# Performance work log

Hardware: AMD Instinct MI355X
Metric: run time of the kernel (lower is better)

## Reference

```python
import jax, jax.numpy as jnp
import numpy as np
import math

VOCAB, D, L, NC, DC, K, DFF = 50257, 1024, 8, 4096, 256, 8, 4096
B, T = 8, 256

def ternary_ste(w):
    # torch: w_q + (w - w_q).detach() -> forward value == w, grad only via w_q
    alpha = jnp.maximum(jnp.mean(jnp.abs(w)), 1e-5)
    w_q = jnp.clip(jnp.round(w / alpha), -1.0, 1.0)
    return w_q + jax.lax.stop_gradient(w - w_q)

def rmsnorm(x, w):
    return x * jax.lax.rsqrt(jnp.mean(x * x, axis=-1, keepdims=True) + 1e-6) * w

def setup_inputs() -> dict:
    key = jax.random.key(0)
    ks = jax.random.split(key, 16)
    n = lambda k, sh, s: (jax.random.normal(k, sh, dtype=jnp.float32) * s)
    return {
        'tokens': jax.random.randint(ks[0], (B, T), 0, VOCAB),
        'embed': n(ks[1], (VOCAB, D), 0.02),
        'ln_in_w': jnp.ones((D,), jnp.float32),
        'ln_out_w': jnp.ones((D,), jnp.float32),
        'W_route': n(ks[2], (L, NC, D), 0.02),
        'cells': n(ks[3], (L, NC, DC), 0.01),
        'W_in': n(ks[4], (L, D, DC), 0.01),
        'W_out': n(ks[5], (L, DC, D), 0.01),
        'state_decay': jnp.full((L,), 3.0, jnp.float32),
        'state_gate_w': jnp.full((L, D), 0.1, jnp.float32),
        'state_gate_b': jnp.zeros((L, D), jnp.float32),
        'state_scale': jnp.full((L, D), 0.1, jnp.float32),
        'cell_scale': jnp.full((L,), 0.1, jnp.float32),
        'W_ff_gate': n(ks[6], (L, D, DFF), 0.02),
        'W_ff_up': n(ks[7], (L, D, DFF), 0.02),
        'W_ff_down': n(ks[8], (L, DFF, D), 0.02),
        'ff_norm_w': jnp.ones((L, D), jnp.float32),
        'norm_w': jnp.ones((L, D), jnp.float32),
    }

def _layer(x, Wr, cells, Wi, Wo, sd, sgw, sgb, ss, cs, Wg, Wu, Wd, ffn_w, nrm_w):
    Bx, Tx, Dx = x.shape
    # cell memory
    scores = jnp.einsum('btd,cd->btc', x, ternary_ste(Wr)) / math.sqrt(Dx)
    topk_s, topk_i = jax.lax.top_k(scores, K)          # [B,T,K]
    w = jax.nn.softmax(topk_s, axis=-1)
    cell_vals = cells[topk_i]                          # [B,T,K,DC]
    readout = jnp.einsum('btkc,btk->btc', cell_vals, w)
    x_in = jnp.einsum('btd,dc->btc', x, ternary_ste(Wi))
    cell_out = jnp.einsum('btc,cd->btd', readout + x_in, ternary_ste(Wo))
    # running state scan
    gate = jax.nn.sigmoid(x * sgw + sgb)
    updates = gate * x                                  # [B,T,D]
    decay = jnp.clip(jax.nn.sigmoid(sd), 0.01, 0.99)
    def step(h, u):
        h = h * decay + u
        return h, h
    _, states = jax.lax.scan(step, jnp.zeros((Bx, Dx), x.dtype), jnp.swapaxes(updates, 0, 1))
    state_out = jnp.swapaxes(states, 0, 1) * ss
    x = rmsnorm(x + cs * cell_out + state_out, nrm_w)
    # ternary SwiGLU FFN
    h = rmsnorm(x, ffn_w)
    g = jnp.einsum('btd,df->btf', h, ternary_ste(Wg))
    u = jnp.einsum('btd,df->btf', h, ternary_ste(Wu))
    ff = jnp.einsum('btf,fd->btd', jax.nn.silu(g) * u, ternary_ste(Wd))
    return x + ff

def reference(tokens, embed, ln_in_w, ln_out_w, W_route, cells, W_in, W_out,
              state_decay, state_gate_w, state_gate_b, state_scale, cell_scale,
              W_ff_gate, W_ff_up, W_ff_down, ff_norm_w, norm_w):
    h = rmsnorm(embed[tokens], ln_in_w)
    for i in range(L):
        h = _layer(h, W_route[i], cells[i], W_in[i], W_out[i], state_decay[i],
                   state_gate_w[i], state_gate_b[i], state_scale[i], cell_scale[i],
                   W_ff_gate[i], W_ff_up[i], W_ff_down[i], ff_norm_w[i], norm_w[i])
    logits = jnp.einsum('btd,vd->btv', rmsnorm(h, ln_out_w), embed)  # tied head
    return logits
```

## Files before the change

kernel.cpp:

```cpp
#include <hip/hip_runtime.h>
#include <stdint.h>

typedef __attribute__((ext_vector_type(8))) short bf16x8;
typedef __attribute__((ext_vector_type(4))) float f32x4;
typedef unsigned short u16;
typedef unsigned int u32;

#define MTOK 2048
#define DMODEL 1024
#define NCELL 4096
#define DCELL 256
#define DFF 4096
#define NVOCAB 50257
#define VPAD_LD 50304

static __device__ __forceinline__ u16 f2bf(float f) {
  u32 u = __builtin_bit_cast(u32, f);
  u = (u + 0x7FFFu + ((u >> 16) & 1u)) >> 16;
  return (u16)u;
}
static __device__ __forceinline__ u32 pk2(float a, float b) {
  return (u32)f2bf(a) | ((u32)f2bf(b) << 16);
}
static __device__ __forceinline__ float sigm(float x) { return 1.0f / (1.0f + __expf(-x)); }

static __device__ __forceinline__ void glds16(const void* g, void* l) {
  __builtin_amdgcn_global_load_lds(
      (const __attribute__((address_space(1))) void*)g,
      (__attribute__((address_space(3))) void*)l, 16, 0, 0);
}

static __device__ __forceinline__ float blockReduceSum(float v) {
#pragma unroll
  for (int o = 32; o > 0; o >>= 1) v += __shfl_xor(v, o);
  __shared__ float sm[4];
  __syncthreads();
  if ((threadIdx.x & 63) == 0) sm[threadIdx.x >> 6] = v;
  __syncthreads();
  return sm[0] + sm[1] + sm[2] + sm[3];
}

static __device__ __forceinline__ float blockReduce1024(float v, float* sm) {
#pragma unroll
  for (int o = 32; o > 0; o >>= 1) v += __shfl_xor(v, o);
  if ((threadIdx.x & 63) == 0) sm[threadIdx.x >> 6] = v;
  __syncthreads();
  float r = 0.f;
#pragma unroll
  for (int i = 0; i < 16; ++i) r += sm[i];
  __syncthreads();
  return r;
}

template<int TM, int TN, int EPI>
__global__ __launch_bounds__(256, 3) void k_gemm_v3(
    const u16* __restrict__ A, const u16* __restrict__ B,
    float* __restrict__ Cf, u16* __restrict__ Cb, const float* __restrict__ Res,
    int NB, int K, int ldc, float alpha)
{
  __shared__ __align__(16) u16 As[TM * 64];
  __shared__ __align__(16) u16 Bs[TN * 64];
  constexpr int MI = TM / 32;
  constexpr int NI = TN / 32;
  constexpr int ACH = TM / 32;
  constexpr int BCH = TN / 32;
  constexpr int MB = 2048 / TM;
  const int tid = threadIdx.x;
  const int T = gridDim.x;
  const int bid = blockIdx.x;
  const int w = (bid & 7) * (T >> 3) + (bid >> 3);
  const int m0 = (w % MB) * TM;
  const int n0 = (w / MB) * TN;
  const int l = tid & 63;
  const int wv = tid >> 6;
  const int wm = wv >> 1, wn = wv & 1;
  const int lr = l & 15, lg = l >> 4;
  const int wbase = tid & ~63;

  f32x4 acc[MI][NI] = {};

  const int row_ = tid >> 3;
  const int kc_ = (tid & 7) << 3;
  const int nk = K >> 6;

  for (int s = 0; s < nk; ++s) {
    const int k0 = s << 6;
#pragma unroll
    for (int c = 0; c < ACH; ++c) {
      int row = c * 32 + row_;
      glds16(&A[(size_t)(m0 + row) * K + k0 + kc_],
             &As[(size_t)(c * 256 + wbase) * 8]);
    }
#pragma unroll
    for (int c = 0; c < BCH; ++c) {
      int row = c * 32 + row_;
      int gr = n0 + row; if (gr > NB - 1) gr = NB - 1;
      glds16(&B[(size_t)gr * K + k0 + kc_],
             &Bs[(size_t)(c * 256 + wbase) * 8]);
    }
    __syncthreads();
#pragma unroll
    for (int kk = 0; kk < 2; ++kk) {
      bf16x8 fa[MI], fb[NI];
#pragma unroll
      for (int mi = 0; mi < MI; ++mi)
        fa[mi] = *(const bf16x8*)&As[(wm * (TM / 2) + mi * 16 + lr) * 64 + kk * 32 + lg * 8];
#pragma unroll
      for (int ni = 0; ni < NI; ++ni)
        fb[ni] = *(const bf16x8*)&Bs[(wn * (TN / 2) + ni * 16 + lr) * 64 + kk * 32 + lg * 8];
#pragma unroll
      for (int mi = 0; mi < MI; ++mi)
#pragma unroll
        for (int ni = 0; ni < NI; ++ni)
          acc[mi][ni] = __builtin_amdgcn_mfma_f32_16x16x32_bf16(fa[mi], fb[ni], acc[mi][ni], 0, 0, 0);
    }
    __syncthreads();
  }

#pragma unroll
  for (int mi = 0; mi < MI; ++mi)
#pragma unroll
    for (int ni = 0; ni < NI; ++ni) {
      int col = n0 + wn * (TN / 2) + ni * 16 + lr;
#pragma unroll
      for (int j = 0; j < 4; ++j) {
        int row = m0 + wm * (TM / 2) + mi * 16 + lg * 4 + j;
        float v = acc[mi][ni][j];
        if constexpr (EPI == 0) {
          Cf[(size_t)row * ldc + col] = v * alpha;
        } else if constexpr (EPI == 1) {
          size_t off = (size_t)row * ldc + col;
          float r = Res[off] + v;
          Cf[off] = r;
          Cb[off] = f2bf(r);
        } else if constexpr (EPI == 2) {
          if (col < NB) Cf[(size_t)row * ldc + col] = v;
        } else if constexpr (EPI == 3) {
          float p = __shfl_xor(v, 1);
          float a = v * sigm(v) * p;
          float a2 = __shfl_xor(a, 2);
          if ((lr & 3) == 0)
            *(u32*)&Cb[(size_t)row * DFF + (col >> 1)] = pk2(a, a2);
        } else {
          __builtin_nontemporal_store(v, &Cf[(size_t)row * ldc + col]);
        }
      }
    }
}

__global__ __launch_bounds__(256) void k_copy_out(
    const float* __restrict__ pad, float* __restrict__ out)
{
  int row = blockIdx.x;
  const float* s = pad + (size_t)row * VPAD_LD;
  float* d = out + (size_t)row * NVOCAB;
  int t = threadIdx.x;
  int head = (int)((16 - (((size_t)d) & 15)) & 15) >> 2;
  if (t < head) d[t] = s[t];
  int nb = (NVOCAB - head) >> 2;
  const float* sb = s + head;
  float* db = d + head;
  for (int i = t; i < nb; i += 256) {
    f32x4 v;
    v.x = __builtin_nontemporal_load(&sb[i * 4 + 0]);
    v.y = __builtin_nontemporal_load(&sb[i * 4 + 1]);
    v.z = __builtin_nontemporal_load(&sb[i * 4 + 2]);
    v.w = __builtin_nontemporal_load(&sb[i * 4 + 3]);
    __builtin_nontemporal_store(v, (f32x4*)&db[i * 4]);
  }
  int t0 = head + nb * 4;
  int rem = NVOCAB - t0;
  if (t < rem) d[t0 + t] = s[t0 + t];
}

static __device__ __forceinline__ void gemm64_body(
    const u16* A, const u16* B, float* Cf,
    int m0, int n0, int K, int lda, int ldb, int ldc, char* smem)
{
  u16* As = (u16*)smem;
  u16* Bs = (u16*)(smem + 64 * 64 * 2);
  const int tid = threadIdx.x;
  const int l = tid & 63;
  const int wv = tid >> 6;
  const int wm = wv >> 1, wn = wv & 1;
  const int lr = l & 15, lg = l >> 4;

  uint4 aR[2], bR[2];
  f32x4 acc[2][2] = {};
  const int nk = K >> 6;

  auto loadAB = [&](int k0) {
#pragma unroll
    for (int c = 0; c < 2; ++c) {
      int id = c * 256 + tid;
      int row = id >> 3, kc = (id & 7) << 3;
      aR[c] = *(const uint4*)&A[(size_t)(m0 + row) * lda + k0 + kc];
      bR[c] = *(const uint4*)&B[(size_t)(n0 + row) * ldb + k0 + kc];
    }
  };
  auto stage = [&]() {
#pragma unroll
    for (int c = 0; c < 2; ++c) {
      int id = c * 256 + tid;
      int row = id >> 3, kc = (id & 7) << 3;
      *(uint4*)&As[row * 64 + kc] = aR[c];
      *(uint4*)&Bs[row * 64 + kc] = bR[c];
    }
  };

  loadAB(0);
  for (int s = 0; s < nk; ++s) {
    __syncthreads();
    stage();
    __syncthreads();
    if (s + 1 < nk) loadAB((s + 1) << 6);
#pragma unroll
    for (int kk = 0; kk < 2; ++kk) {
      bf16x8 fa[2], fb[2];
#pragma unroll
      for (int mi = 0; mi < 2; ++mi)
        fa[mi] = *(const bf16x8*)&As[(wm * 32 + mi * 16 + lr) * 64 + kk * 32 + lg * 8];
#pragma unroll
      for (int ni = 0; ni < 2; ++ni)
        fb[ni] = *(const bf16x8*)&Bs[(wn * 32 + ni * 16 + lr) * 64 + kk * 32 + lg * 8];
#pragma unroll
      for (int mi = 0; mi < 2; ++mi)
#pragma unroll
        for (int ni = 0; ni < 2; ++ni)
          acc[mi][ni] = __builtin_amdgcn_mfma_f32_16x16x32_bf16(fa[mi], fb[ni], acc[mi][ni], 0, 0, 0);
    }
  }

#pragma unroll
  for (int mi = 0; mi < 2; ++mi)
#pragma unroll
    for (int ni = 0; ni < 2; ++ni) {
      int col = n0 + wn * 32 + ni * 16 + lr;
#pragma unroll
      for (int j = 0; j < 4; ++j) {
        int row = m0 + wm * 32 + mi * 16 + lg * 4 + j;
        Cf[(size_t)row * ldc + col] = acc[mi][ni][j];
      }
    }
}

__global__ __launch_bounds__(256, 3) void k_gemm64(
    const u16* __restrict__ A, const u16* __restrict__ B,
    float* __restrict__ Cf, int K, int lda, int ldb, int ldc)
{
  __shared__ __align__(16) char smem[16384];
  gemm64_body(A, B, Cf, blockIdx.x * 64, blockIdx.y * 64, K, lda, ldb, ldc, smem);
}

__global__ __launch_bounds__(256, 3) void k_prep_fused(
    const u16* __restrict__ x_bf, const u16* __restrict__ WiT,
    float* __restrict__ xin,
    const float* __restrict__ x_f, float* __restrict__ E,
    const float* __restrict__ sgw, const float* __restrict__ sgb,
    const float* __restrict__ sdec)
{
  __shared__ __align__(16) char smem[16384];
  int bid = blockIdx.x;
  if (bid < 128) {
    gemm64_body(x_bf, WiT, xin, (bid & 31) * 64, (bid >> 5) * 64,
                DMODEL, DMODEL, DMODEL, DCELL, smem);
    return;
  }
  int tid = (bid - 128) * 256 + threadIdx.x;
  int d = tid & 1023, bc = tid >> 10;
  int b = bc >> 4, c = bc & 15;
  float dec = sigm(sdec[0]);
  dec = fminf(fmaxf(dec, 0.01f), 0.99f);
  float gw = sgw[d], gb = sgb[d];
  size_t base = ((size_t)b * 256 + c * 16) * DMODEL + d;
  float h = 0.f;
  for (int t = 0; t < 16; ++t) {
    float xv = x_f[base + (size_t)t * DMODEL];
    h = h * dec + sigm(xv * gw + gb) * xv;
  }
  E[tid] = h;
}

__global__ __launch_bounds__(256) void k_cell_fused(
    const float* __restrict__ scores, const float* __restrict__ cells,
    const float* __restrict__ xin, u16* __restrict__ rb)
{
  __shared__ float sw[4][8];
  __shared__ int si[4][8];
  int row0 = blockIdx.x * 4;
  int wvid = threadIdx.x >> 6;
  int row = row0 + wvid;
  int l = threadIdx.x & 63;
  const float* s = scores + (size_t)row * NCELL;
  float v[8]; int ix[8];
#pragma unroll
  for (int i = 0; i < 8; ++i) { v[i] = -3.4e38f; ix[i] = 0x7fffffff; }
  for (int j = 0; j < 64; ++j) {
    float x = s[j * 64 + l];
    if (x > v[7]) {
      v[7] = x; ix[7] = j * 64 + l;
#pragma unroll
      for (int q = 7; q > 0; --q) {
        if (v[q] > v[q - 1]) {
          float tv = v[q]; v[q] = v[q - 1]; v[q - 1] = tv;
          int tt = ix[q]; ix[q] = ix[q - 1]; ix[q - 1] = tt;
        }
      }
    }
  }
  float ov[8]; int oi[8];
#pragma unroll
  for (int r = 0; r < 8; ++r) {
    float bv = v[0]; int bi = ix[0];
#pragma unroll
    for (int o = 32; o > 0; o >>= 1) {
      float tv = __shfl_xor(bv, o);
      int tb = __shfl_xor(bi, o);
      if (tv > bv || (tv == bv && tb < bi)) { bv = tv; bi = tb; }
    }
    ov[r] = bv; oi[r] = bi;
    if (bi == ix[0]) {
#pragma unroll
      for (int q = 0; q < 7; ++q) { v[q] = v[q + 1]; ix[q] = ix[q + 1]; }
      v[7] = -3.4e38f; ix[7] = 0x7fffffff;
    }
  }
  if (l == 0) {
    float m = ov[0], sum = 0.f, e[8];
#pragma unroll
    for (int r = 0; r < 8; ++r) { e[r] = __expf(ov[r] - m); sum += e[r]; }
    float inv = 1.0f / sum;
#pragma unroll
    for (int r = 0; r < 8; ++r) { sw[wvid][r] = e[r] * inv; si[wvid][r] = oi[r]; }
  }
  __syncthreads();
  int d = threadIdx.x;
#pragma unroll
  for (int r = 0; r < 4; ++r) {
    int rr = row0 + r;
    float acc = xin[(size_t)rr * DCELL + d];
#pragma unroll
    for (int k = 0; k < 8; ++k)
      acc += sw[r][k] * cells[(size_t)si[r][k] * DCELL + d];
    rb[(size_t)rr * DCELL + d] = f2bf(acc);
  }
}

__global__ __launch_bounds__(1024) void k_scan_norm(
    float* __restrict__ x_f, const float* __restrict__ co,
    const float* __restrict__ E, u16* __restrict__ h2b,
    const float* __restrict__ sgw, const float* __restrict__ sgb,
    const float* __restrict__ ssc, const float* __restrict__ sdec,
    const float* __restrict__ csc, const float* __restrict__ nw,
    const float* __restrict__ fw)
{
  __shared__ float sm[16];
  int b = blockIdx.x >> 4, c = blockIdx.x & 15;
  int d = threadIdx.x;
  float dec = sigm(sdec[0]);
  dec = fminf(fmaxf(dec, 0.01f), 0.99f);
  float d2 = dec * dec, d4 = d2 * d2, d8 = d4 * d4;
  float d16 = d8 * d8;
  float cs = csc[0];
  float gw = sgw[d], gb = sgb[d], sc = ssc[d];
  float nwd = nw[d], fwd = fw[d];
  float h = 0.f;
  for (int cc = 0; cc < c; ++cc) h = h * d16 + E[((b << 4) + cc) * 1024 + d];
  size_t base = ((size_t)b * 256 + c * 16) * DMODEL + d;
  for (int t = 0; t < 16; ++t) {
    size_t o = base + (size_t)t * DMODEL;
    float xv = x_f[o];
    float g = sigm(xv * gw + gb);
    h = h * dec + g * xv;
    float pre = xv + cs * co[o] + h * sc;
    float s1 = blockReduce1024(pre * pre, sm);
    float inv = rsqrtf(s1 * (1.0f / DMODEL) + 1e-6f);
    float x1 = pre * inv * nwd;
    float s2 = blockReduce1024(x1 * x1, sm);
    float inv2 = rsqrtf(s2 * (1.0f / DMODEL) + 1e-6f);
    x_f[o] = x1;
    h2b[o] = f2bf(x1 * inv2 * fwd);
  }
}

__global__ void k_transpose_layer(
    const float* __restrict__ Wi, const float* __restrict__ Wo,
    const float* __restrict__ Wg, const float* __restrict__ Wu,
    const float* __restrict__ Wd, const float* __restrict__ Wr,
    u16* __restrict__ WiT, u16* __restrict__ WoT,
    u16* __restrict__ WguT, u16* __restrict__ WdT, u16* __restrict__ WrB)
{
  int bid = blockIdx.x;
  if (bid >= 12800) {
    int i = (bid - 12800) * 256 + threadIdx.x;
    const float4* s = (const float4*)(Wr + (size_t)i * 8);
    float4 a = s[0], b = s[1];
    *(uint4*)(WrB + (size_t)i * 8) =
        make_uint4(pk2(a.x, a.y), pk2(a.z, a.w), pk2(b.x, b.y), pk2(b.z, b.w));
    return;
  }
  const float* src; u16* dst; int R, C, t0, mul, add;
  if (bid < 256)       { src = Wi; dst = WiT;  R = 1024; C = 256;  t0 = bid;        mul = 1; add = 0; }
  else if (bid < 512)  { src = Wo; dst = WoT;  R = 256;  C = 1024; t0 = bid - 256;  mul = 1; add = 0; }
  else if (bid < 4608) { src = Wg; dst = WguT; R = 1024; C = 4096; t0 = bid - 512;  mul = 2; add = 0; }
  else if (bid < 8704) { src = Wu; dst = WguT; R = 1024; C = 4096; t0 = bid - 4608; mul = 2; add = 1; }
  else                 { src = Wd; dst = WdT;  R = 4096; C = 1024; t0 = bid - 8704; mul = 1; add = 0; }
  int tC = C >> 5;
  int r0 = (t0 / tC) << 5, c0 = (t0 % tC) << 5;
  __shared__ float tile[32][33];
  int ty = threadIdx.x >> 3;
  int tx = (threadIdx.x & 7) << 2;
  float4 v = *(const float4*)&src[(size_t)(r0 + ty) * C + c0 + tx];
  tile[ty][tx] = v.x; tile[ty][tx + 1] = v.y; tile[ty][tx + 2] = v.z; tile[ty][tx + 3] = v.w;
  __syncthreads();
  float a = tile[tx][ty], b = tile[tx + 1][ty], c = tile[tx + 2][ty], d = tile[tx + 3][ty];
  *(uint2*)&dst[((size_t)(c0 + ty) * mul + add) * R + r0 + tx] = make_uint2(pk2(a, b), pk2(c, d));
}

__global__ void k_embed_norm(const int* __restrict__ tok, const float* __restrict__ emb,
                             const float* __restrict__ w, float* __restrict__ xf,
                             u16* __restrict__ xb)
{
  int row = blockIdx.x;
  int t = tok[row];
  float4 v = ((const float4*)(emb + (size_t)t * DMODEL))[threadIdx.x];
  float tot = blockReduceSum(v.x * v.x + v.y * v.y + v.z * v.z + v.w * v.w);
  float inv = rsqrtf(tot * (1.0f / DMODEL) + 1e-6f);
  int d0 = threadIdx.x << 2;
  float4 wv = *(const float4*)(w + d0);
  float4 o;
  o.x = v.x * inv * wv.x; o.y = v.y * inv * wv.y;
  o.z = v.z * inv * wv.z; o.w = v.w * inv * wv.w;
  *(float4*)(xf + (size_t)row * DMODEL + d0) = o;
  *(uint2*)(xb + (size_t)row * DMODEL + d0) = make_uint2(pk2(o.x, o.y), pk2(o.z, o.w));
}

__global__ __launch_bounds__(256) void k_tail(
    const float* __restrict__ xf, const float* __restrict__ w,
    u16* __restrict__ ob, const float* __restrict__ emb,
    u16* __restrict__ emb_bf)
{
  int bid = blockIdx.x;
  if (bid >= 2048) {
    int i = (bid - 2048) * 256 + threadIdx.x;
    if (i >= NVOCAB * (DMODEL / 8)) return;
    const float4* s = (const float4*)(emb + (size_t)i * 8);
    float4 a = s[0], b = s[1];
    *(uint4*)(emb_bf + (size_t)i * 8) =
        make_uint4(pk2(a.x, a.y), pk2(a.z, a.w), pk2(b.x, b.y), pk2(b.z, b.w));
    return;
  }
  int row = bid;
  float4 v = ((const float4*)(xf + (size_t)row * DMODEL))[threadIdx.x];
  float tot = blockReduceSum(v.x * v.x + v.y * v.y + v.z * v.z + v.w * v.w);
  float inv = rsqrtf(tot * (1.0f / DMODEL) + 1e-6f);
  int d0 = threadIdx.x << 2;
  float4 wv = *(const float4*)(w + d0);
  *(uint2*)(ob + (size_t)row * DMODEL + d0) =
      make_uint2(pk2(v.x * inv * wv.x, v.y * inv * wv.y),
                 pk2(v.z * inv * wv.z, v.w * inv * wv.w));
}

extern "C" void kernel_launch(void* const* d_in, const int* in_sizes, int n_in,
                              void* d_out, int out_size, void* d_ws, size_t ws_size,
                              hipStream_t stream)
{
  const int*   tokens  = (const int*)d_in[0];
  const float* embed   = (const float*)d_in[1];
  const float* ln_in_w = (const float*)d_in[2];
  const float* ln_out_w= (const float*)d_in[3];
  const float* W_route = (const float*)d_in[4];
  const float* cells   = (const float*)d_in[5];
  const float* W_in    = (const float*)d_in[6];
  const float* W_out   = (const float*)d_in[7];
  const float* sdec    = (const float*)d_in[8];
  const float* sgw     = (const float*)d_in[9];
  const float* sgb     = (const float*)d_in[10];
  const float* ssc     = (const float*)d_in[11];
  const float* csc     = (const float*)d_in[12];
  const float* Wg      = (const float*)d_in[13];
  const float* Wu      = (const float*)d_in[14];
  const float* Wd      = (const float*)d_in[15];
  const float* ffw     = (const float*)d_in[16];
  const float* nrw     = (const float*)d_in[17];
  float* out = (float*)d_out;
  (void)in_sizes; (void)n_in; (void)out_size;

  char* ws = (char*)d_ws;
  size_t off = 0;
  auto alloc = [&](size_t bytes) -> void* {
    void* p = ws + off;
    off += (bytes + 255) & ~(size_t)255;
    return p;
  };

  float* scores = (float*)alloc((size_t)MTOK * NCELL * 4);
  u16*  act_bf  = (u16*)alloc((size_t)MTOK * DFF * 2);
  float* x_f    = (float*)alloc((size_t)MTOK * DMODEL * 4);
  u16*  x_bf    = (u16*)alloc((size_t)MTOK * DMODEL * 2);
  u16*  h2_bf   = (u16*)alloc((size_t)MTOK * DMODEL * 2);
  float* xin    = (float*)alloc((size_t)MTOK * DCELL * 4);
  u16*  r_bf    = (u16*)alloc((size_t)MTOK * DCELL * 2);
  float* cellout= (float*)alloc((size_t)MTOK * DMODEL * 4);
  u16*  WiT     = (u16*)alloc((size_t)DCELL * DMODEL * 2);
  u16*  WoT     = (u16*)alloc((size_t)DMODEL * DCELL * 2);
  u16*  WguT    = (u16*)alloc((size_t)8192 * DMODEL * 2);
  u16*  WdT     = (u16*)alloc((size_t)DMODEL * DFF * 2);
  u16*  WrB     = (u16*)alloc((size_t)NCELL * DMODEL * 2);
  float* E      = (float*)alloc((size_t)131072 * 4);
  if (off < ((size_t)108 << 20)) off = (size_t)108 << 20;
  u16*  xf_bf   = (u16*)alloc((size_t)MTOK * DMODEL * 2);
  float* vpad   = (float*)alloc((size_t)MTOK * VPAD_LD * 4);
  size_t need_pad = off;
  u16*  embed_bf = (u16*)ws;

  const bool use_pad = (ws_size >= need_pad);

  k_embed_norm<<<MTOK, 256, 0, stream>>>(tokens, embed, ln_in_w, x_f, x_bf);

  for (int lay = 0; lay < 8; ++lay) {
    const float* Wi_l = W_in  + (size_t)lay * DMODEL * DCELL;
    const float* Wo_l = W_out + (size_t)lay * DCELL * DMODEL;
    const float* Wg_l = Wg    + (size_t)lay * DMODEL * DFF;
    const float* Wu_l = Wu    + (size_t)lay * DMODEL * DFF;
    const float* Wd_l = Wd    + (size_t)lay * DFF * DMODEL;
    const float* Wr_l = W_route + (size_t)lay * NCELL * DMODEL;
    const float* cells_l = cells + (size_t)lay * NCELL * DCELL;

    k_transpose_layer<<<14848, 256, 0, stream>>>(Wi_l, Wo_l, Wg_l, Wu_l, Wd_l,
                                                 Wr_l, WiT, WoT, WguT, WdT, WrB);
    k_gemm_v3<128, 128, 0><<<512, 256, 0, stream>>>(x_bf, WrB, scores, nullptr,
        nullptr, NCELL, DMODEL, NCELL, 0.03125f);
    k_prep_fused<<<640, 256, 0, stream>>>(x_bf, WiT, xin, x_f, E,
        sgw + lay * DMODEL, sgb + lay * DMODEL, sdec + lay);
    k_cell_fused<<<512, 256, 0, stream>>>(scores, cells_l, xin, r_bf);
    k_gemm64<<<dim3(32, 16), 256, 0, stream>>>(r_bf, WoT, cellout,
        DCELL, DCELL, DCELL, DMODEL);
    k_scan_norm<<<128, 1024, 0, stream>>>(x_f, cellout, E, h2_bf,
        sgw + lay * DMODEL, sgb + lay * DMODEL, ssc + lay * DMODEL,
        sdec + lay, csc + lay, nrw + lay * DMODEL, ffw + lay * DMODEL);
    k_gemm_v3<128, 128, 3><<<1024, 256, 0, stream>>>(h2_bf, WguT, nullptr, act_bf,
        nullptr, 8192, DMODEL, 0, 1.0f);
    k_gemm_v3<64, 64, 1><<<512, 256, 0, stream>>>(act_bf, WdT, x_f, x_bf, x_f,
        DMODEL, DFF, DMODEL, 1.0f);
  }

  k_tail<<<2048 + 25129, 256, 0, stream>>>(x_f, ln_out_w, xf_bf, embed, embed_bf);
  if (use_pad) {
    k_gemm_v3<128, 64, 4><<<12576, 256, 0, stream>>>(xf_bf, embed_bf, vpad, nullptr,
        nullptr, NVOCAB, DMODEL, VPAD_LD, 1.0f);
    k_copy_out<<<MTOK, 256, 0, stream>>>(vpad, out);
  } else {
    k_gemm_v3<128, 64, 2><<<12576, 256, 0, stream>>>(xf_bf, embed_bf, out, nullptr,
        nullptr, NVOCAB, DMODEL, NVOCAB, 1.0f);
  }
}
```

Measured before the change: 2.779 ms.

## Overlap next-layer weight transpose with down-proj GEMM and enlarge logits tile

Fuses the next layer's weight transpose/bf16 conversion into the same launch as the current layer's down-projection GEMM. Extra blocks do the conversion while GEMM blocks run, and WdT is double-buffered to avoid a hazard. This hides the separate per-layer transpose launch, which is bandwidth-bound, behind compute. The tied-head logits GEMM also moves from a 128x64 to a 128x128 tile. One risk is that WiT/WguT/WrB get overwritten while the earlier kernels of the same layer are done; the stream ordering keeps that safe.

```diff
diff --git a/kernel.cpp b/kernel.cpp
--- a/kernel.cpp
+++ b/kernel.cpp
@@ -53,21 +53,20 @@
 }
 
 template<int TM, int TN, int EPI>
-__global__ __launch_bounds__(256, 3) void k_gemm_v3(
-    const u16* __restrict__ A, const u16* __restrict__ B,
-    float* __restrict__ Cf, u16* __restrict__ Cb, const float* __restrict__ Res,
+static __device__ __forceinline__ void v3_body(
+    int bid, int T, char* smem,
+    const u16* A, const u16* B,
+    float* Cf, u16* Cb, const float* Res,
     int NB, int K, int ldc, float alpha)
 {
-  __shared__ __align__(16) u16 As[TM * 64];
-  __shared__ __align__(16) u16 Bs[TN * 64];
+  u16* As = (u16*)smem;
+  u16* Bs = (u16*)(smem + TM * 128);
   constexpr int MI = TM / 32;
   constexpr int NI = TN / 32;
   constexpr int ACH = TM / 32;
   constexpr int BCH = TN / 32;
   constexpr int MB = 2048 / TM;
   const int tid = threadIdx.x;
-  const int T = gridDim.x;
-  const int bid = blockIdx.x;
   const int w = (bid & 7) * (T >> 3) + (bid >> 3);
   const int m0 = (w % MB) * TM;
   const int n0 = (w / MB) * TN;
@@ -146,6 +145,81 @@
         }
       }
     }
+}
+
+template<int TM, int TN, int EPI>
+__global__ __launch_bounds__(256, 3) void k_gemm_v3(
+    const u16* __restrict__ A, const u16* __restrict__ B,
+    float* __restrict__ Cf, u16* __restrict__ Cb, const float* __restrict__ Res,
+    int NB, int K, int ldc, float alpha)
+{
+  __shared__ __align__(16) char smem[(TM + TN) * 128];
+  v3_body<TM, TN, EPI>(blockIdx.x, gridDim.x, smem, A, B, Cf, Cb, Res,
+                       NB, K, ldc, alpha);
+}
+
+static __device__ __forceinline__ void transpose_body(
+    int bid, char* smem,
+    const float* Wi, const float* Wo, const float* Wg, const float* Wu,
+    const float* Wd, const float* Wr,
+    u16* WiT, u16* WoT, u16* WguT, u16* WdT, u16* WrB)
+{
+  if (bid >= 12800) {
+    int i = (bid - 12800) * 256 + threadIdx.x;
+    const float4* s = (const float4*)(Wr + (size_t)i * 8);
+    float4 a = s[0], b = s[1];
+    *(uint4*)(WrB + (size_t)i * 8) =
+        make_uint4(pk2(a.x, a.y), pk2(a.z, a.w), pk2(b.x, b.y), pk2(b.z, b.w));
+    return;
+  }
+  const float* src; u16* dst; int R, C, t0, mul, add;
+  if (bid < 256)       { src = Wi; dst = WiT;  R = 1024; C = 256;  t0 = bid;        mul = 1; add = 0; }
+  else if (bid < 512)  { src = Wo; dst = WoT;  R = 256;  C = 1024; t0 = bid - 256;  mul = 1; add = 0; }
+  else if (bid < 4608) { src = Wg; dst = WguT; R = 1024; C = 4096; t0 = bid - 512;  mul = 2; add = 0; }
+  else if (bid < 8704) { src = Wu; dst = WguT; R = 1024; C = 4096; t0 = bid - 4608; mul = 2; add = 1; }
+  else                 { src = Wd; dst = WdT;  R = 4096; C = 1024; t0 = bid - 8704; mul = 1; add = 0; }
+  int tC = C >> 5;
+  int r0 = (t0 / tC) << 5, c0 = (t0 % tC) << 5;
+  float (*tile)[33] = (float(*)[33])smem;
+  int ty = threadIdx.x >> 3;
+  int tx = (threadIdx.x & 7) << 2;
+  float4 v = *(const float4*)&src[(size_t)(r0 + ty) * C + c0 + tx];
+  tile[ty][tx] = v.x; tile[ty][tx + 1] = v.y; tile[ty][tx + 2] = v.z; tile[ty][tx + 3] = v.w;
+  __syncthreads();
+  float a = tile[tx][ty], b = tile[tx + 1][ty], c = tile[tx + 2][ty], d = tile[tx + 3][ty];
+  *(uint2*)&dst[((size_t)(c0 + ty) * mul + add) * R + r0 + tx] = make_uint2(pk2(a, b), pk2(c, d));
+}
+
+__global__ void k_transpose_layer(
+    const float* __restrict__ Wi, const float* __restrict__ Wo,
+    const float* __restrict__ Wg, const float* __restrict__ Wu,
+    const float* __restrict__ Wd, const float* __restrict__ Wr,
+    u16* __restrict__ WiT, u16* __restrict__ WoT,
+    u16* __restrict__ WguT, u16* __restrict__ WdT, u16* __restrict__ WrB)
+{
+  __shared__ __align__(16) char smem[4224];
+  transpose_body(blockIdx.x, smem, Wi, Wo, Wg, Wu, Wd, Wr,
+                 WiT, WoT, WguT, WdT, WrB);
+}
+
+__global__ __launch_bounds__(256, 3) void k_wd_prep(
+    const u16* __restrict__ act, const u16* __restrict__ WdT_cur,
+    float* __restrict__ x_f, u16* __restrict__ x_bf,
+    const float* __restrict__ Wi, const float* __restrict__ Wo,
+    const float* __restrict__ Wg, const float* __restrict__ Wu,
+    const float* __restrict__ Wd, const float* __restrict__ Wr,
+    u16* __restrict__ WiT, u16* __restrict__ WoT,
+    u16* __restrict__ WguT, u16* __restrict__ WdT_nxt, u16* __restrict__ WrB)
+{
+  __shared__ __align__(16) char smem[16384];
+  int bid = blockIdx.x;
+  if (bid < 512) {
+    v3_body<64, 64, 1>(bid, 512, smem, act, WdT_cur, x_f, x_bf, x_f,
+                       DMODEL, DFF, DMODEL, 1.0f);
+  } else {
+    transpose_body(bid - 512, smem, Wi, Wo, Wg, Wu, Wd, Wr,
+                   WiT, WoT, WguT, WdT_nxt, WrB);
+  }
 }
 
 __global__ __launch_bounds__(256) void k_copy_out(
@@ -383,40 +457,6 @@
   }
 }
 
-__global__ void k_transpose_layer(
-    const float* __restrict__ Wi, const float* __restrict__ Wo,
-    const float* __restrict__ Wg, const float* __restrict__ Wu,
-    const float* __restrict__ Wd, const float* __restrict__ Wr,
-    u16* __restrict__ WiT, u16* __restrict__ WoT,
-    u16* __restrict__ WguT, u16* __restrict__ WdT, u16* __restrict__ WrB)
-{
-  int bid = blockIdx.x;
-  if (bid >= 12800) {
-    int i = (bid - 12800) * 256 + threadIdx.x;
-    const float4* s = (const float4*)(Wr + (size_t)i * 8);
-    float4 a = s[0], b = s[1];
-    *(uint4*)(WrB + (size_t)i * 8) =
-        make_uint4(pk2(a.x, a.y), pk2(a.z, a.w), pk2(b.x, b.y), pk2(b.z, b.w));
-    return;
-  }
-  const float* src; u16* dst; int R, C, t0, mul, add;
-  if (bid < 256)       { src = Wi; dst = WiT;  R = 1024; C = 256;  t0 = bid;        mul = 1; add = 0; }
-  else if (bid < 512)  { src = Wo; dst = WoT;  R = 256;  C = 1024; t0 = bid - 256;  mul = 1; add = 0; }
-  else if (bid < 4608) { src = Wg; dst = WguT; R = 1024; C = 4096; t0 = bid - 512;  mul = 2; add = 0; }
-  else if (bid < 8704) { src = Wu; dst = WguT; R = 1024; C = 4096; t0 = bid - 4608; mul = 2; add = 1; }
-  else                 { src = Wd; dst = WdT;  R = 4096; C = 1024; t0 = bid - 8704; mul = 1; add = 0; }
-  int tC = C >> 5;
-  int r0 = (t0 / tC) << 5, c0 = (t0 % tC) << 5;
-  __shared__ float tile[32][33];
-  int ty = threadIdx.x >> 3;
-  int tx = (threadIdx.x & 7) << 2;
-  float4 v = *(const float4*)&src[(size_t)(r0 + ty) * C + c0 + tx];
-  tile[ty][tx] = v.x; tile[ty][tx + 1] = v.y; tile[ty][tx + 2] = v.z; tile[ty][tx + 3] = v.w;
-  __syncthreads();
-  float a = tile[tx][ty], b = tile[tx + 1][ty], c = tile[tx + 2][ty], d = tile[tx + 3][ty];
-  *(uint2*)&dst[((size_t)(c0 + ty) * mul + add) * R + r0 + tx] = make_uint2(pk2(a, b), pk2(c, d));
-}
-
 __global__ void k_embed_norm(const int* __restrict__ tok, const float* __restrict__ emb,
                              const float* __restrict__ w, float* __restrict__ xf,
                              u16* __restrict__ xb)
@@ -505,7 +545,8 @@
   u16*  WiT     = (u16*)alloc((size_t)DCELL * DMODEL * 2);
   u16*  WoT     = (u16*)alloc((size_t)DMODEL * DCELL * 2);
   u16*  WguT    = (u16*)alloc((size_t)8192 * DMODEL * 2);
-  u16*  WdT     = (u16*)alloc((size_t)DMODEL * DFF * 2);
+  u16*  WdTa    = (u16*)alloc((size_t)DMODEL * DFF * 2);
+  u16*  WdTb    = (u16*)alloc((size_t)DMODEL * DFF * 2);
   u16*  WrB     = (u16*)alloc((size_t)NCELL * DMODEL * 2);
   float* E      = (float*)alloc((size_t)131072 * 4);
   if (off < ((size_t)108 << 20)) off = (size_t)108 << 20;
@@ -517,18 +558,14 @@
   const bool use_pad = (ws_size >= need_pad);
 
   k_embed_norm<<<MTOK, 256, 0, stream>>>(tokens, embed, ln_in_w, x_f, x_bf);
+  k_transpose_layer<<<14848, 256, 0, stream>>>(W_in, W_out, Wg, Wu, Wd, W_route,
+                                               WiT, WoT, WguT, WdTa, WrB);
 
   for (int lay = 0; lay < 8; ++lay) {
-    const float* Wi_l = W_in  + (size_t)lay * DMODEL * DCELL;
-    const float* Wo_l = W_out + (size_t)lay * DCELL * DMODEL;
-    const float* Wg_l = Wg    + (size_t)lay * DMODEL * DFF;
-    const float* Wu_l = Wu    + (size_t)lay * DMODEL * DFF;
-    const float* Wd_l = Wd    + (size_t)lay * DFF * DMODEL;
-    const float* Wr_l = W_route + (size_t)lay * NCELL * DMODEL;
     const float* cells_l = cells + (size_t)lay * NCELL * DCELL;
-
-    k_transpose_layer<<<14848, 256, 0, stream>>>(Wi_l, Wo_l, Wg_l, Wu_l, Wd_l,
-                                                 Wr_l, WiT, WoT, WguT, WdT, WrB);
+    u16* WdT_cur = (lay & 1) ? WdTb : WdTa;
+    u16* WdT_nxt = (lay & 1) ? WdTa : WdTb;
+
     k_gemm_v3<128, 128, 0><<<512, 256, 0, stream>>>(x_bf, WrB, scores, nullptr,
         nullptr, NCELL, DMODEL, NCELL, 0.03125f);
     k_prep_fused<<<640, 256, 0, stream>>>(x_bf, WiT, xin, x_f, E,
@@ -541,17 +578,29 @@
         sdec + lay, csc + lay, nrw + lay * DMODEL, ffw + lay * DMODEL);
     k_gemm_v3<128, 128, 3><<<1024, 256, 0, stream>>>(h2_bf, WguT, nullptr, act_bf,
         nullptr, 8192, DMODEL, 0, 1.0f);
-    k_gemm_v3<64, 64, 1><<<512, 256, 0, stream>>>(act_bf, WdT, x_f, x_bf, x_f,
-        DMODEL, DFF, DMODEL, 1.0f);
+    if (lay < 7) {
+      int nl = lay + 1;
+      k_wd_prep<<<15360, 256, 0, stream>>>(act_bf, WdT_cur, x_f, x_bf,
+          W_in  + (size_t)nl * DMODEL * DCELL,
+          W_out + (size_t)nl * DCELL * DMODEL,
+          Wg    + (size_t)nl * DMODEL * DFF,
+          Wu    + (size_t)nl * DMODEL * DFF,
+          Wd    + (size_t)nl * DFF * DMODEL,
+          W_route + (size_t)nl * NCELL * DMODEL,
+          WiT, WoT, WguT, WdT_nxt, WrB);
+    } else {
+      k_gemm_v3<64, 64, 1><<<512, 256, 0, stream>>>(act_bf, WdT_cur, x_f, x_bf,
+          x_f, DMODEL, DFF, DMODEL, 1.0f);
+    }
   }
 
   k_tail<<<2048 + 25129, 256, 0, stream>>>(x_f, ln_out_w, xf_bf, embed, embed_bf);
   if (use_pad) {
-    k_gemm_v3<128, 64, 4><<<12576, 256, 0, stream>>>(xf_bf, embed_bf, vpad, nullptr,
+    k_gemm_v3<128, 128, 4><<<6288, 256, 0, stream>>>(xf_bf, embed_bf, vpad, nullptr,
         nullptr, NVOCAB, DMODEL, VPAD_LD, 1.0f);
     k_copy_out<<<MTOK, 256, 0, stream>>>(vpad, out);
   } else {
-    k_gemm_v3<128, 64, 2><<<12576, 256, 0, stream>>>(xf_bf, embed_bf, out, nullptr,
+    k_gemm_v3<128, 128, 2><<<6288, 256, 0, stream>>>(xf_bf, embed_bf, out, nullptr,
         nullptr, NVOCAB, DMODEL, NVOCAB, 1.0f);
   }
 }
```

Result: faster. 2.664 ms (-4.1%).
